# Optimization experiments

Hardware: AMD Instinct MI355X
Metric: run time of the kernel (lower is better)

The kernel has to match this reference:

```python
import jax, jax.numpy as jnp
import numpy as np

H = 768
I = 3072
E = 8
B, S = 2, 512
EPS = 1e-12


def setup_inputs() -> dict:
    key = jax.random.key(0)
    ks = jax.random.split(key, 8)
    hidden_states = jax.random.normal(ks[0], (B, S, H), dtype=jnp.float32)
    expert_idx = jax.random.randint(ks[1], (B * S,), 0, E)
    scale1 = 1.0 / np.sqrt(H)
    scale2 = 1.0 / np.sqrt(I)
    W1 = jax.random.uniform(ks[2], (E, H, I), jnp.float32, -scale1, scale1)
    b1 = jax.random.uniform(ks[3], (E, I), jnp.float32, -scale1, scale1)
    W2 = jax.random.uniform(ks[4], (E, I, H), jnp.float32, -scale2, scale2)
    b2 = jax.random.uniform(ks[5], (E, H), jnp.float32, -scale2, scale2)
    gamma = jnp.ones((H,), jnp.float32)
    beta = jnp.zeros((H,), jnp.float32)
    return {
        "hidden_states": hidden_states,
        "expert_idx": expert_idx,
        "W1": W1, "b1": b1, "W2": W2, "b2": b2,
        "gamma": gamma, "beta": beta,
    }


def _moe_ln(hidden_states, expert_idx, W1, b1, W2, b2, gamma, beta):
    b, s, h = hidden_states.shape
    x = hidden_states.reshape(-1, h)  # [T, H]
    out = jnp.zeros_like(x)
    # loop over the small fixed expert count; select per-token results by mask
    for e in range(E):
        inter = jax.nn.gelu(x @ W1[e] + b1[e], approximate=False)
        y_e = inter @ W2[e] + b2[e]
        out = jnp.where((expert_idx == e)[:, None], y_e, out)
    y = out.reshape(b, s, h) + hidden_states  # residual
    mu = jnp.mean(y, axis=-1, keepdims=True)
    var = jnp.mean(jnp.square(y - mu), axis=-1, keepdims=True)
    return (y - mu) * jax.lax.rsqrt(var + EPS) * gamma + beta


def reference(hidden_states, expert_idx, W1, b1, W2, b2, gamma, beta):
    return _moe_ln(hidden_states, expert_idx, W1, b1, W2, b2, gamma, beta)
```

## Files before the change

### kernel.cpp

```cpp
#include <hip/hip_runtime.h>
#include <math.h>

#define T_TOK 1024
#define H_DIM 768
#define I_DIM 3072
#define E_NUM 8
#define BM    128
#define BN    64
#define BK    64
#define MSLOTS 16
#define KSPLIT2 4

typedef __attribute__((ext_vector_type(8))) short  short8;
typedef __attribute__((ext_vector_type(4))) float  f32x4;

__device__ __forceinline__ unsigned short f2bf(float f) {
  union { float f; unsigned u; } a; a.f = f;
  unsigned r = a.u + 0x7FFFu + ((a.u >> 16) & 1u);
  return (unsigned short)(r >> 16);
}
__device__ __forceinline__ float gelu_exact(float x) {
  return 0.5f * x * (1.0f + erff(x * 0.70710678118654752f));
}
__device__ __forceinline__ int swz(int row, int k) {
  return row * BK + (k ^ ((row & 7) << 3));
}
__device__ __forceinline__ void gll16(const void* g, void* l) {
  __builtin_amdgcn_global_load_lds(
      (const __attribute__((address_space(1))) void*)g,
      (__attribute__((address_space(3))) void*)l, 16, 0, 0);
}

__global__ __launch_bounds__(1024) void route_kernel(
    const int* __restrict__ eidx, int* __restrict__ perm,
    int* __restrict__ tile_e, int* __restrict__ tile_row,
    int* __restrict__ tile_len, int* __restrict__ ntiles) {
  __shared__ int wcnt[16][E_NUM];
  __shared__ int wpre[16][E_NUM];
  __shared__ int offsh[E_NUM + 1];
  const int t = threadIdx.x;
  const int lane = t & 63, wave = t >> 6;
  const int e = eidx[t];
  unsigned long long myMask = 0;
#pragma unroll
  for (int ee = 0; ee < E_NUM; ++ee) {
    unsigned long long m = __ballot(e == ee);
    if (ee == e) myMask = m;
    if (lane == 0) wcnt[wave][ee] = __popcll(m);
  }
  const int rank = __popcll(myMask & ((1ull << lane) - 1ull));
  __syncthreads();
  if (t < 16 * E_NUM) {
    const int w = t >> 3, ee = t & 7;
    int p = 0;
    for (int w2 = 0; w2 < w; ++w2) p += wcnt[w2][ee];
    wpre[w][ee] = p;
  }
  __syncthreads();
  if (t <= E_NUM) {
    int off = 0;
    for (int ee = 0; ee < t; ++ee) off += wpre[15][ee] + wcnt[15][ee];
    offsh[t] = off;
  }
  __syncthreads();
  perm[offsh[e] + wpre[wave][e] + rank] = t;
  if (t == 0) {
    int n = 0;
    for (int ee = 0; ee < E_NUM; ++ee)
      for (int r = offsh[ee]; r < offsh[ee + 1]; r += BM) {
        tile_e[n] = ee; tile_row[n] = r;
        tile_len[n] = min(offsh[ee + 1] - r, BM); ++n;
      }
    *ntiles = n;
    for (int i = n; i < MSLOTS; ++i) { tile_e[i] = 0; tile_row[i] = 0; tile_len[i] = 0; }
  }
}

__global__ void gather_kernel(const float* __restrict__ x,
                              const int* __restrict__ perm,
                              unsigned short* __restrict__ xg) {
  const int idx = blockIdx.x * 256 + threadIdx.x;
  if (idx >= T_TOK * (H_DIM / 8)) return;
  const int p = idx / (H_DIM / 8);
  const int c = (idx % (H_DIM / 8)) * 8;
  const int t = perm[p];
  const float* src = x + (size_t)t * H_DIM + c;
  const float4 v0 = *(const float4*)(src);
  const float4 v1 = *(const float4*)(src + 4);
  short8 o;
  o[0] = (short)f2bf(v0.x); o[1] = (short)f2bf(v0.y);
  o[2] = (short)f2bf(v0.z); o[3] = (short)f2bf(v0.w);
  o[4] = (short)f2bf(v1.x); o[5] = (short)f2bf(v1.y);
  o[6] = (short)f2bf(v1.z); o[7] = (short)f2bf(v1.w);
  *(short8*)(xg + (size_t)p * H_DIM + c) = o;
}

template <int N_FULL, int K_FULL, int KLOOP, bool IS_FFN1>
__global__ __launch_bounds__(512, 4) void moe_gemm(
    const unsigned short* __restrict__ A,
    const float* __restrict__ W,
    const float* __restrict__ bias,
    const int* __restrict__ tile_e, const int* __restrict__ tile_row,
    const int* __restrict__ tile_len, const int* __restrict__ ntiles,
    unsigned short* __restrict__ out_bf,
    float* __restrict__ part) {
  constexpr int KT = KLOOP / BK;
  const int tid  = threadIdx.x;
  const int slot = blockIdx.y;
  if (slot >= *ntiles) return;
  const int e    = tile_e[slot];
  const int row0 = tile_row[slot];
  const int len  = tile_len[slot];
  const int n0   = blockIdx.x * BN;
  const int kbase = blockIdx.z * KLOOP;
  const float* We = W + (size_t)e * K_FULL * N_FULL;

  __shared__ unsigned short As[2][BM * BK];
  __shared__ unsigned short Bs[2][BN * BK];

  const int lane = tid & 63;
  const int wave = tid >> 6;
  const int wm = wave >> 1, wn = wave & 1;
  const int lr = lane & 15;
  const int lk = (lane >> 4) * 8;

  const unsigned short* agsrc[2];
  int aoff[2];
#pragma unroll
  for (int i = 0; i < 2; ++i) {
    const int c = tid + i * 512;
    const int r = c >> 3, kc = (c & 7) << 3;
    int grow = row0 + r; grow = grow < T_TOK ? grow : (T_TOK - 1);
    agsrc[i] = A + (size_t)grow * K_FULL + kbase + (kc ^ ((r & 7) << 3));
    aoff[i]  = ((tid & ~63) + i * 512) * 8;
  }
  const int bn_ = tid & 63;
  const int kb8 = (tid >> 6) * 8;
  const float* wpB = We + (size_t)(kbase + kb8) * N_FULL + n0 + bn_;

  f32x4 acc[2][2] = {};
  float X[8], Y[8];

  auto issueA = [&](int kt, int buf) {
#pragma unroll
    for (int i = 0; i < 2; ++i)
      gll16(agsrc[i] + kt * BK, &As[buf][aoff[i]]);
  };
  auto loadB = [&](int kt, float* d) {
#pragma unroll
    for (int j = 0; j < 8; ++j)
      d[j] = wpB[(size_t)(kt * BK + j) * N_FULL];
  };
  auto writeB = [&](int buf, const float* d) {
    short8 p;
#pragma unroll
    for (int j = 0; j < 8; ++j) p[j] = (short)f2bf(d[j]);
    *(short8*)(&Bs[buf][swz(bn_, kb8)]) = p;
  };
  auto mfma_tile = [&](int buf) {
#pragma unroll
    for (int ks = 0; ks < 2; ++ks) {
      const int kp = ks * 32 + lk;
      short8 af[2], bfr[2];
#pragma unroll
      for (int m = 0; m < 2; ++m)
        af[m] = *(const short8*)(&As[buf][swz(wm * 32 + m * 16 + lr, kp)]);
#pragma unroll
      for (int n = 0; n < 2; ++n)
        bfr[n] = *(const short8*)(&Bs[buf][swz(wn * 32 + n * 16 + lr, kp)]);
#pragma unroll
      for (int m = 0; m < 2; ++m)
#pragma unroll
        for (int n = 0; n < 2; ++n)
          acc[m][n] = __builtin_amdgcn_mfma_f32_16x16x32_bf16(af[m], bfr[n], acc[m][n], 0, 0, 0);
    }
  };
  auto phase = [&](int t, int buf, float* setCur, bool nextA, bool nextB, bool drain) {
    if (drain) asm volatile("s_waitcnt vmcnt(0)" ::: "memory");
    else       asm volatile("s_waitcnt vmcnt(8)" ::: "memory");
    writeB(buf, setCur);
    asm volatile("s_waitcnt lgkmcnt(0)" ::: "memory");
    __builtin_amdgcn_s_barrier();
    __builtin_amdgcn_sched_barrier(0);
    if (nextA) issueA(t + 1, buf ^ 1);
    __builtin_amdgcn_sched_barrier(0);
    if (nextB) loadB(t + 2, setCur);
    __builtin_amdgcn_sched_barrier(0);
    mfma_tile(buf);
  };

  loadB(0, X);
  __builtin_amdgcn_sched_barrier(0);
  issueA(0, 0);
  __builtin_amdgcn_sched_barrier(0);
  loadB(1, Y);
#pragma unroll 1
  for (int t = 0; t < KT - 2; t += 2) {
    phase(t,     0, X, true, true, false);
    phase(t + 1, 1, Y, true, true, false);
  }
  phase(KT - 2, 0, X, true,  false, false);
  phase(KT - 1, 1, Y, false, false, true);

#pragma unroll
  for (int n = 0; n < 2; ++n) {
    const int gc = n0 + wn * 32 + n * 16 + lr;
    float bv = 0.f;
    if constexpr (IS_FFN1) bv = bias[(size_t)e * N_FULL + gc];
#pragma unroll
    for (int m = 0; m < 2; ++m) {
      const int rbase = wm * 32 + m * 16 + (lane >> 4) * 4;
#pragma unroll
      for (int j = 0; j < 4; ++j) {
        const int rl = rbase + j;
        if (rl < len) {
          if constexpr (IS_FFN1) {
            out_bf[(size_t)(row0 + rl) * N_FULL + gc] = f2bf(gelu_exact(acc[m][n][j] + bv));
          } else {
            part[((size_t)blockIdx.z * T_TOK + row0 + rl) * N_FULL + gc] = acc[m][n][j];
          }
        }
      }
    }
  }
}

__global__ void ln_kernel(const float* __restrict__ part,
                          const float* __restrict__ x,
                          const int* __restrict__ perm,
                          const int* __restrict__ eidx,
                          const float* __restrict__ b2,
                          const float* __restrict__ gamma,
                          const float* __restrict__ beta,
                          float* __restrict__ out) {
  const int p = blockIdx.x;
  const int tid = threadIdx.x;
  const int t = perm[p];
  const int e = eidx[t];
  float v[3], s = 0.f, ss = 0.f;
#pragma unroll
  for (int i = 0; i < 3; ++i) {
    const int c = tid + i * 256;
    float a = x[(size_t)t * H_DIM + c] + b2[(size_t)e * H_DIM + c];
#pragma unroll
    for (int s4 = 0; s4 < KSPLIT2; ++s4)
      a += part[((size_t)s4 * T_TOK + p) * H_DIM + c];
    v[i] = a; s += a; ss += a * a;
  }
#pragma unroll
  for (int o = 32; o; o >>= 1) { s += __shfl_down(s, o); ss += __shfl_down(ss, o); }
  __shared__ float ps[4], pss[4];
  __shared__ float mu_s, ir_s;
  const int w = tid >> 6;
  if ((tid & 63) == 0) { ps[w] = s; pss[w] = ss; }
  __syncthreads();
  if (tid == 0) {
    const float S = ps[0] + ps[1] + ps[2] + ps[3];
    const float SS = pss[0] + pss[1] + pss[2] + pss[3];
    const float mu = S * (1.0f / H_DIM);
    const float var = SS * (1.0f / H_DIM) - mu * mu;
    mu_s = mu; ir_s = rsqrtf(var + 1e-12f);
  }
  __syncthreads();
  const float mu = mu_s, ir = ir_s;
#pragma unroll
  for (int i = 0; i < 3; ++i) {
    const int c = tid + i * 256;
    out[(size_t)t * H_DIM + c] = (v[i] - mu) * ir * gamma[c] + beta[c];
  }
}

extern "C" void kernel_launch(void* const* d_in, const int* in_sizes, int n_in,
                              void* d_out, int out_size, void* d_ws, size_t ws_size,
                              hipStream_t stream) {
  const float* x     = (const float*)d_in[0];
  const int*   eidx  = (const int*)d_in[1];
  const float* W1    = (const float*)d_in[2];
  const float* b1    = (const float*)d_in[3];
  const float* W2    = (const float*)d_in[4];
  const float* b2    = (const float*)d_in[5];
  const float* gamma = (const float*)d_in[6];
  const float* beta  = (const float*)d_in[7];
  float* out = (float*)d_out;

  char* ws = (char*)d_ws;
  int* perm     = (int*)(ws);
  int* tile_e   = (int*)(ws + 4096);
  int* tile_row = (int*)(ws + 4352);
  int* tile_len = (int*)(ws + 4608);
  int* ntiles   = (int*)(ws + 4864);
  size_t off = 8192;
  unsigned short* xg = (unsigned short*)(ws + off);  off += (size_t)2 * T_TOK * H_DIM;
  unsigned short* inter = (unsigned short*)(ws + off); off += (size_t)2 * T_TOK * I_DIM;
  float* part = (float*)(ws + off);

  route_kernel<<<1, T_TOK, 0, stream>>>(eidx, perm, tile_e, tile_row, tile_len, ntiles);
  gather_kernel<<<(T_TOK * (H_DIM / 8) + 255) / 256, 256, 0, stream>>>(x, perm, xg);
  moe_gemm<I_DIM, H_DIM, H_DIM, true>
      <<<dim3(I_DIM / BN, MSLOTS, 1), 512, 0, stream>>>(
      xg, W1, b1, tile_e, tile_row, tile_len, ntiles, inter, nullptr);
  moe_gemm<H_DIM, I_DIM, I_DIM / KSPLIT2, false>
      <<<dim3(H_DIM / BN, MSLOTS, KSPLIT2), 512, 0, stream>>>(
      inter, W2, nullptr, tile_e, tile_row, tile_len, ntiles, nullptr, part);
  ln_kernel<<<T_TOK, 256, 0, stream>>>(part, x, perm, eidx, b2, gamma, beta, out);
  (void)in_sizes; (void)n_in; (void)out_size; (void)ws_size;
}
```

Baseline: 76.00 us.

## Pre-convert weights to tiled bf16 and stream them with direct LDS loads

Adds conversion kernels that, on every call, transpose and convert the fp32 W1/W2 into a swizzled bf16 tile layout in workspace. New GEMM kernels then load both A and B tiles with direct global-to-LDS copies in a 3-stage pipeline, which removes the per-thread fp32 load and bf16 conversion from the GEMM inner loop. In exchange it adds a full extra read and write pass over both weight tensors each call. The new path runs only when the workspace is large enough, and the old kernels are kept as a fallback.

Measured after the change: 112.0 us. 47.4% more time.

```diff
diff --git a/kernel.cpp b/kernel.cpp
--- a/kernel.cpp
+++ b/kernel.cpp
@@ -95,8 +95,143 @@
   *(short8*)(xg + (size_t)p * H_DIM + c) = o;
 }
 
+template <int KROWS, int NCOLS, int TPS>
+__global__ __launch_bounds__(512) void conv_kernel(
+    const float* __restrict__ W, unsigned short* __restrict__ Wt) {
+  constexpr int KTT = KROWS / 64, NP = NCOLS / 64;
+  __shared__ unsigned short lds[TPS * 4096];
+  const int kt = blockIdx.x, nG = blockIdx.y, e = blockIdx.z;
+  const int t = threadIdx.x;
+  const float* src = W + ((size_t)e * KROWS + kt * 64) * NCOLS + nG * (TPS * 64);
+#pragma unroll
+  for (int i = 0; i < TPS * 2; ++i) {
+    const int idx = i * 512 + t;
+    const int r = idx / (TPS * 16);
+    const int c4 = (idx % (TPS * 16)) * 4;
+    const float4 v = *(const float4*)(src + (size_t)r * NCOLS + c4);
+#pragma unroll
+    for (int j = 0; j < 4; ++j) {
+      const int n = c4 + j;
+      lds[(n >> 6) * 4096 + (n & 63) * 64 + (r ^ ((n & 7) << 3))] = f2bf((&v.x)[j]);
+    }
+  }
+  __syncthreads();
+  unsigned short* dst = Wt + ((size_t)(e * NP + nG * TPS) * KTT + kt) * 4096;
+#pragma unroll
+  for (int tc = 0; tc < TPS; ++tc)
+    *(short8*)(dst + (size_t)tc * KTT * 4096 + t * 8) =
+        *(const short8*)(&lds[tc * 4096 + t * 8]);
+}
+
 template <int N_FULL, int K_FULL, int KLOOP, bool IS_FFN1>
-__global__ __launch_bounds__(512, 4) void moe_gemm(
+__global__ __launch_bounds__(512, 4) void moe_gemm_t(
+    const unsigned short* __restrict__ A,
+    const unsigned short* __restrict__ Wt,
+    const float* __restrict__ bias,
+    const int* __restrict__ tile_e, const int* __restrict__ tile_row,
+    const int* __restrict__ tile_len, const int* __restrict__ ntiles,
+    unsigned short* __restrict__ out_bf,
+    float* __restrict__ part) {
+  constexpr int KT  = KLOOP / BK;
+  constexpr int NP  = N_FULL / 64, KTT = K_FULL / 64;
+  const int tid  = threadIdx.x;
+  const int slot = blockIdx.y;
+  if (slot >= *ntiles) return;
+  const int e    = tile_e[slot];
+  const int row0 = tile_row[slot];
+  const int len  = tile_len[slot];
+  const int n0   = blockIdx.x * BN;
+  const int ktbase = blockIdx.z * KT;
+
+  __shared__ unsigned short As[3][BM * BK];
+  __shared__ unsigned short Bs[3][BN * BK];
+
+  const int lane = tid & 63;
+  const int wave = tid >> 6;
+  const int wm = wave >> 1, wn = wave & 1;
+  const int lr = lane & 15;
+  const int lk = (lane >> 4) * 8;
+
+  const unsigned short* agsrc[2];
+  int aoff[2];
+#pragma unroll
+  for (int i = 0; i < 2; ++i) {
+    const int c = tid + i * 512;
+    const int r = c >> 3, kc = (c & 7) << 3;
+    int grow = row0 + r; grow = grow < T_TOK ? grow : (T_TOK - 1);
+    agsrc[i] = A + (size_t)grow * K_FULL + ktbase * BK + (kc ^ ((r & 7) << 3));
+    aoff[i]  = ((tid & ~63) + i * 512) * 8;
+  }
+  const unsigned short* btile =
+      Wt + ((size_t)(e * NP + blockIdx.x) * KTT + ktbase) * 4096 + wave * 512 + lane * 8;
+  const int boff = wave * 512;
+
+  f32x4 acc[2][2] = {};
+
+  auto issue = [&](int t, int b) {
+#pragma unroll
+    for (int i = 0; i < 2; ++i)
+      gll16(agsrc[i] + t * BK, &As[b][aoff[i]]);
+    gll16(btile + (size_t)t * 4096, &Bs[b][boff]);
+  };
+  auto mfma_tile = [&](int b) {
+#pragma unroll
+    for (int ks = 0; ks < 2; ++ks) {
+      const int kpos = ks * 32 + lk;
+      short8 af[2], bfr[2];
+#pragma unroll
+      for (int m = 0; m < 2; ++m)
+        af[m] = *(const short8*)(&As[b][swz(wm * 32 + m * 16 + lr, kpos)]);
+#pragma unroll
+      for (int n = 0; n < 2; ++n)
+        bfr[n] = *(const short8*)(&Bs[b][swz(wn * 32 + n * 16 + lr, kpos)]);
+#pragma unroll
+      for (int m = 0; m < 2; ++m)
+#pragma unroll
+        for (int n = 0; n < 2; ++n)
+          acc[m][n] = __builtin_amdgcn_mfma_f32_16x16x32_bf16(af[m], bfr[n], acc[m][n], 0, 0, 0);
+    }
+  };
+
+  issue(0, 0);
+  issue(1, 1);
+#pragma unroll 1
+  for (int t = 0; t < KT; ++t) {
+    const int b = t % 3;
+    if (t == KT - 1) asm volatile("s_waitcnt vmcnt(0)" ::: "memory");
+    else             asm volatile("s_waitcnt vmcnt(3)" ::: "memory");
+    __builtin_amdgcn_s_barrier();
+    __builtin_amdgcn_sched_barrier(0);
+    if (t + 2 < KT) issue(t + 2, (t + 2) % 3);
+    __builtin_amdgcn_sched_barrier(0);
+    mfma_tile(b);
+  }
+
+#pragma unroll
+  for (int n = 0; n < 2; ++n) {
+    const int gc = n0 + wn * 32 + n * 16 + lr;
+    float bv = 0.f;
+    if constexpr (IS_FFN1) bv = bias[(size_t)e * N_FULL + gc];
+#pragma unroll
+    for (int m = 0; m < 2; ++m) {
+      const int rbase = wm * 32 + m * 16 + (lane >> 4) * 4;
+#pragma unroll
+      for (int j = 0; j < 4; ++j) {
+        const int rl = rbase + j;
+        if (rl < len) {
+          if constexpr (IS_FFN1) {
+            out_bf[(size_t)(row0 + rl) * N_FULL + gc] = f2bf(gelu_exact(acc[m][n][j] + bv));
+          } else {
+            part[((size_t)blockIdx.z * T_TOK + row0 + rl) * N_FULL + gc] = acc[m][n][j];
+          }
+        }
+      }
+    }
+  }
+}
+
+template <int N_FULL, int K_FULL, int KLOOP, bool IS_FFN1>
+__global__ __launch_bounds__(512, 4) void moe_gemm_f(
     const unsigned short* __restrict__ A,
     const float* __restrict__ W,
     const float* __restrict__ bias,
@@ -114,16 +249,13 @@
   const int n0   = blockIdx.x * BN;
   const int kbase = blockIdx.z * KLOOP;
   const float* We = W + (size_t)e * K_FULL * N_FULL;
-
   __shared__ unsigned short As[2][BM * BK];
   __shared__ unsigned short Bs[2][BN * BK];
-
   const int lane = tid & 63;
   const int wave = tid >> 6;
   const int wm = wave >> 1, wn = wave & 1;
   const int lr = lane & 15;
   const int lk = (lane >> 4) * 8;
-
   const unsigned short* agsrc[2];
   int aoff[2];
 #pragma unroll
@@ -137,10 +269,8 @@
   const int bn_ = tid & 63;
   const int kb8 = (tid >> 6) * 8;
   const float* wpB = We + (size_t)(kbase + kb8) * N_FULL + n0 + bn_;
-
   f32x4 acc[2][2] = {};
   float X[8], Y[8];
-
   auto issueA = [&](int kt, int buf) {
 #pragma unroll
     for (int i = 0; i < 2; ++i)
@@ -188,7 +318,6 @@
     __builtin_amdgcn_sched_barrier(0);
     mfma_tile(buf);
   };
-
   loadB(0, X);
   __builtin_amdgcn_sched_barrier(0);
   issueA(0, 0);
@@ -201,7 +330,6 @@
   }
   phase(KT - 2, 0, X, true,  false, false);
   phase(KT - 1, 1, Y, false, false, true);
-
 #pragma unroll
   for (int n = 0; n < 2; ++n) {
     const int gc = n0 + wn * 32 + n * 16 + lr;
@@ -290,18 +418,33 @@
   int* tile_len = (int*)(ws + 4608);
   int* ntiles   = (int*)(ws + 4864);
   size_t off = 8192;
-  unsigned short* xg = (unsigned short*)(ws + off);  off += (size_t)2 * T_TOK * H_DIM;
+  unsigned short* xg = (unsigned short*)(ws + off);    off += (size_t)2 * T_TOK * H_DIM;
   unsigned short* inter = (unsigned short*)(ws + off); off += (size_t)2 * T_TOK * I_DIM;
-  float* part = (float*)(ws + off);
+  float* part = (float*)(ws + off);                    off += (size_t)4 * KSPLIT2 * T_TOK * H_DIM;
+  unsigned short* w1t = (unsigned short*)(ws + off);   off += (size_t)2 * E_NUM * H_DIM * I_DIM;
+  unsigned short* w2t = (unsigned short*)(ws + off);
+  const size_t need = off + (size_t)2 * E_NUM * H_DIM * I_DIM;
+  const bool tiled = ws_size >= need;
 
   route_kernel<<<1, T_TOK, 0, stream>>>(eidx, perm, tile_e, tile_row, tile_len, ntiles);
   gather_kernel<<<(T_TOK * (H_DIM / 8) + 255) / 256, 256, 0, stream>>>(x, perm, xg);
-  moe_gemm<I_DIM, H_DIM, H_DIM, true>
-      <<<dim3(I_DIM / BN, MSLOTS, 1), 512, 0, stream>>>(
-      xg, W1, b1, tile_e, tile_row, tile_len, ntiles, inter, nullptr);
-  moe_gemm<H_DIM, I_DIM, I_DIM / KSPLIT2, false>
-      <<<dim3(H_DIM / BN, MSLOTS, KSPLIT2), 512, 0, stream>>>(
-      inter, W2, nullptr, tile_e, tile_row, tile_len, ntiles, nullptr, part);
+  if (tiled) {
+    conv_kernel<H_DIM, I_DIM, 8><<<dim3(H_DIM / 64, I_DIM / 512, E_NUM), 512, 0, stream>>>(W1, w1t);
+    conv_kernel<I_DIM, H_DIM, 6><<<dim3(I_DIM / 64, H_DIM / 384, E_NUM), 512, 0, stream>>>(W2, w2t);
+    moe_gemm_t<I_DIM, H_DIM, H_DIM, true>
+        <<<dim3(I_DIM / BN, MSLOTS, 1), 512, 0, stream>>>(
+        xg, w1t, b1, tile_e, tile_row, tile_len, ntiles, inter, nullptr);
+    moe_gemm_t<H_DIM, I_DIM, I_DIM / KSPLIT2, false>
+        <<<dim3(H_DIM / BN, MSLOTS, KSPLIT2), 512, 0, stream>>>(
+        inter, w2t, nullptr, tile_e, tile_row, tile_len, ntiles, nullptr, part);
+  } else {
+    moe_gemm_f<I_DIM, H_DIM, H_DIM, true>
+        <<<dim3(I_DIM / BN, MSLOTS, 1), 512, 0, stream>>>(
+        xg, W1, b1, tile_e, tile_row, tile_len, ntiles, inter, nullptr);
+    moe_gemm_f<H_DIM, I_DIM, I_DIM / KSPLIT2, false>
+        <<<dim3(H_DIM / BN, MSLOTS, KSPLIT2), 512, 0, stream>>>(
+        inter, W2, nullptr, tile_e, tile_row, tile_len, ntiles, nullptr, part);
+  }
   ln_kernel<<<T_TOK, 256, 0, stream>>>(part, x, perm, eidx, b2, gamma, beta, out);
-  (void)in_sizes; (void)n_in; (void)out_size; (void)ws_size;
-}
+  (void)in_sizes; (void)n_in; (void)out_size;
+}
```
